# Kernel optimization log

Hardware: AMD Instinct MI355X
Metric: run time of the kernel (lower is better)

## Reference

```python
import jax, jax.numpy as jnp
import numpy as np

B, H, W, C = 16, 64, 64, 256
DIRECTIONS = [(0, -1), (1, -1), (1, 0), (1, 1), (0, 1), (-1, 1), (-1, 0), (-1, -1)]


def _shift(g, dx, dy):
    # zero-padded shift matching the torch _shift_grid semantics:
    # result[:, max(0,dy):H+min(0,dy), max(0,dx):W+min(0,dx)] = g[src slices]
    _, h, w, _ = g.shape
    padded = jnp.pad(g, ((0, 0), (max(0, dy), max(0, -dy)), (max(0, dx), max(0, -dx)), (0, 0)))
    return padded[:, max(0, -dy):max(0, -dy) + h, max(0, -dx):max(0, -dx) + w, :]


def setup_inputs() -> dict:
    key = jax.random.key(0)
    k1, k2, k3, k4 = jax.random.split(key, 4)
    grid_embedding = jax.random.normal(k1, (B, H, W, C), dtype=jnp.float32)
    Wd = jax.random.normal(k2, (8, C, C), dtype=jnp.float32) * 0.01  # per-direction weights
    Wc = jax.random.normal(k3, (C, 8 * C), dtype=jnp.float32) * 0.02  # Linear weight [out, in]
    bc = jax.random.normal(k4, (C,), dtype=jnp.float32) * 0.02
    return {"grid_embedding": grid_embedding, "Wd": Wd, "Wc": Wc, "bc": bc}


def reference(grid_embedding, Wd, Wc, bc):
    # stack the 8 zero-padded shifted copies: [8, B, H, W, C]
    shifted = jnp.stack([_shift(grid_embedding, dx, dy) for (dx, dy) in DIRECTIONS], axis=0)
    # per-direction channel matmul: [B, H, W, 8, C] (d-major over last two dims matches torch.cat order)
    proc = jnp.einsum('dbhwc,dce->bhwde', shifted, Wd)
    combined = proc.reshape(grid_embedding.shape[0], grid_embedding.shape[1], grid_embedding.shape[2], -1)
    # nn.Linear: y = x @ W.T + b
    return combined @ Wc.T + bc
```

## Files before the change

### kernel.cpp

```cpp
#include <hip/hip_runtime.h>


typedef unsigned short u16;
typedef unsigned int u32;
typedef __attribute__((ext_vector_type(8))) short bf16x8;
typedef __attribute__((ext_vector_type(4))) float f32x4;

#define GP_BYTES 35684352

__device__ __forceinline__ u16 f2bf(float f) {
  u32 u = __float_as_uint(f);
  u32 r = u + 0x7fffu + ((u >> 16) & 1u);
  return (u16)(r >> 16);
}
__device__ __forceinline__ u32 pack2(float a, float b) {
  return (u32)f2bf(a) | ((u32)f2bf(b) << 16);
}

__global__ __launch_bounds__(256) void pad_convert(const float* __restrict__ g,
                                                   u16* __restrict__ gp) {
  int id = blockIdx.x * 256 + threadIdx.x;
  if (id >= 2230272) return;
  int c8 = id & 31;
  int t = id >> 5;
  int xx = t % 66;
  int s = t / 66;
  int yy = s % 66;
  int b  = s / 66;
  u32 o0 = 0, o1 = 0, o2 = 0, o3 = 0;
  if (yy != 0 && yy != 65 && xx != 0 && xx != 65) {
    const float* src = g + ((((b << 6) + yy - 1) << 6) + xx - 1) * 256 + (c8 << 3);
    float4 fa = *(const float4*)src;
    float4 fb = *(const float4*)(src + 4);
    o0 = pack2(fa.x, fa.y);
    o1 = pack2(fa.z, fa.w);
    o2 = pack2(fb.x, fb.y);
    o3 = pack2(fb.z, fb.w);
  }
  uint4 v; v.x = o0; v.y = o1; v.z = o2; v.w = o3;
  *(uint4*)(gp + (size_t)id * 8) = v;
}

__global__ __launch_bounds__(256) void build_mt(const float* __restrict__ Wd,
                                                const float* __restrict__ Wc,
                                                u16* __restrict__ Bf) {
  __shared__ __align__(16) u16 As[128 * 32];
  __shared__ __align__(16) u16 Bs[128 * 32];
  const int bid = blockIdx.x;
  const int n0    = (bid & 1) << 7;
  const int mblk  = bid >> 1;
  const int d     = mblk >> 1;
  const int chalf = (mblk & 1) << 7;
  const int tid  = threadIdx.x;
  const int lane = tid & 63, wid = tid >> 6;
  const int wm = (wid >> 1) << 6, wn = (wid & 1) << 6;
  const int quad = lane >> 4, r16 = lane & 15;
  const int srow = tid >> 1, hh = tid & 1;
  const int swz  = (srow >> 1) & 3;
  const int ssl  = (quad ^ ((r16 >> 1) & 3)) << 3;
  f32x4 acc[4][4] = {};

  for (int e0 = 0; e0 < 256; e0 += 32) {
    __syncthreads();
    const float* pa = Wd + (size_t)(d * 256 + chalf + srow) * 256 + e0 + hh * 16;
    const float* pb = Wc + (size_t)(n0 + srow) * 2048 + d * 256 + e0 + hh * 16;
#pragma unroll
    for (int i = 0; i < 2; ++i) {
      float4 a0 = *(const float4*)(pa + i * 8);
      float4 a1 = *(const float4*)(pa + i * 8 + 4);
      float4 b0 = *(const float4*)(pb + i * 8);
      float4 b1 = *(const float4*)(pb + i * 8 + 4);
      uint4 va, vb;
      va.x = pack2(a0.x, a0.y); va.y = pack2(a0.z, a0.w);
      va.z = pack2(a1.x, a1.y); va.w = pack2(a1.z, a1.w);
      vb.x = pack2(b0.x, b0.y); vb.y = pack2(b0.z, b0.w);
      vb.z = pack2(b1.x, b1.y); vb.w = pack2(b1.z, b1.w);
      int slot = (2 * hh + i) ^ swz;
      *(uint4*)&As[srow * 32 + slot * 8] = va;
      *(uint4*)&Bs[srow * 32 + slot * 8] = vb;
    }
    __syncthreads();
    bf16x8 bfr[4];
#pragma unroll
    for (int nt = 0; nt < 4; ++nt)
      bfr[nt] = *(const bf16x8*)&Bs[(wn + nt * 16 + r16) * 32 + ssl];
#pragma unroll
    for (int mt = 0; mt < 4; ++mt) {
      bf16x8 af = *(const bf16x8*)&As[(wm + mt * 16 + r16) * 32 + ssl];
#pragma unroll
      for (int nt = 0; nt < 4; ++nt)
        acc[mt][nt] = __builtin_amdgcn_mfma_f32_16x16x32_bf16(af, bfr[nt], acc[mt][nt], 0, 0, 0);
    }
  }
#pragma unroll
  for (int mt = 0; mt < 4; ++mt) {
#pragma unroll
    for (int nt = 0; nt < 4; ++nt) {
      const int o = n0 + wn + nt * 16 + r16;
      f32x4 v = acc[mt][nt];
#pragma unroll
      for (int r = 0; r < 4; ++r) {
        const int c = chalf + wm + mt * 16 + quad * 4 + r;
        const int lane2 = (o & 15) + (((c >> 3) & 3) << 4);
        const size_t idx = ((size_t)((d * 8 + (c >> 5)) * 16 + (o >> 4)) * 512) + lane2 * 8 + (c & 7);
        Bf[idx] = f2bf(v[r]);
      }
    }
  }
}

__constant__ int DOFF[8] = {16896, 16640, -256, -17152, -16896, -16640, 256, 17152};

__device__ __forceinline__ void async16(const u16* g, u16* l) {
  __builtin_amdgcn_global_load_lds((const __attribute__((address_space(1))) u32*)g,
                                   (__attribute__((address_space(3))) u32*)l, 16, 0, 0);
}

__global__ __launch_bounds__(512, 2) void conv_gemm(const u16* __restrict__ gp,
                                                    const u16* __restrict__ Bf,
                                                    const float* __restrict__ bc,
                                                    float* __restrict__ out) {
  __shared__ __align__(16) u16 Asm[4][8192];
  const int bid = blockIdx.x;
  const int id2 = ((bid & 7) << 5) | (bid >> 3);
  const int b   = id2 >> 4;
  const int y0  = (id2 & 15) << 2;

  const int tid  = threadIdx.x;
  const int lane = tid & 63;
  const int wid  = tid >> 6;
  const int wm   = (wid >> 2) << 7;
  const int wn   = (wid & 3) << 6;
  const int quad = lane >> 4;
  const int r16  = lane & 15;

  const int chunk = (tid & 3) ^ ((tid >> 3) & 3);
  const u16* baseA = gp + ((b * 66 + y0 + 1 + (tid >> 8)) * 66 + ((tid >> 2) & 63) + 1) * 256
                        + (chunk << 3);
  const int ldso = tid * 8;

  const u16* baseBf = Bf + (wn >> 4) * 512 + lane * 8;

  const int ssl = (quad ^ ((r16 >> 1) & 3)) << 3;

  f32x4 acc[8][4] = {};
  bf16x8 bcur[4], bnxt[4];

  auto issueA = [&](int kt) {
    const int off = DOFF[kt >> 3] + ((kt & 7) << 5);
    async16(baseA + off,         Asm[kt & 3] + ldso);
    async16(baseA + off + 33792, Asm[kt & 3] + 4096 + ldso);
  };
  auto loadB = [&](int kt, bf16x8* dst) {
    const u16* bp = baseBf + (size_t)kt * 8192;
#pragma unroll
    for (int nt = 0; nt < 4; ++nt) dst[nt] = *(const bf16x8*)(bp + nt * 512);
  };
  auto readA = [&](int kt, bf16x8* af) {
    const u16* Ab = Asm[kt & 3];
#pragma unroll
    for (int mt = 0; mt < 8; ++mt)
      af[mt] = *(const bf16x8*)&Ab[(wm + mt * 16 + r16) * 32 + ssl];
  };
  auto domfma = [&](const bf16x8* af, const bf16x8* bb) {
    __builtin_amdgcn_s_setprio(1);
#pragma unroll
    for (int mt = 0; mt < 8; ++mt)
#pragma unroll
      for (int nt = 0; nt < 4; ++nt)
        acc[mt][nt] = __builtin_amdgcn_mfma_f32_16x16x32_bf16(af[mt], bb[nt], acc[mt][nt], 0, 0, 0);
    __builtin_amdgcn_s_setprio(0);
  };

  loadB(0, bcur);
  issueA(0);
  issueA(1);
  asm volatile("s_waitcnt vmcnt(2)" ::: "memory");
  asm volatile("s_barrier" ::: "memory");

#pragma unroll 2
  for (int kt = 0; kt < 62; ++kt) {
    loadB(kt + 1, bnxt);
    bf16x8 af[8];
    readA(kt, af);
    issueA(kt + 2);
    domfma(af, bcur);
    asm volatile("s_waitcnt vmcnt(2)" ::: "memory");
    asm volatile("s_barrier" ::: "memory");
#pragma unroll
    for (int nt = 0; nt < 4; ++nt) bcur[nt] = bnxt[nt];
  }
  {
    loadB(63, bnxt);
    bf16x8 af[8];
    readA(62, af);
    domfma(af, bcur);
    asm volatile("s_waitcnt vmcnt(0)" ::: "memory");
    asm volatile("s_barrier" ::: "memory");
#pragma unroll
    for (int nt = 0; nt < 4; ++nt) bcur[nt] = bnxt[nt];
  }
  {
    bf16x8 af[8];
    readA(63, af);
    domfma(af, bcur);
  }

  const int pbase = (b * 64 + y0) * 64;
#pragma unroll
  for (int nt = 0; nt < 4; ++nt) {
    const int o = wn + nt * 16 + r16;
    const float bias = bc[o];
#pragma unroll
    for (int mt = 0; mt < 8; ++mt) {
      const int pr = pbase + wm + mt * 16 + quad * 4;
      f32x4 v = acc[mt][nt];
#pragma unroll
      for (int r = 0; r < 4; ++r)
        out[(size_t)(pr + r) * 256 + o] = v[r] + bias;
    }
  }
}

extern "C" void kernel_launch(void* const* d_in, const int* in_sizes, int n_in,
                              void* d_out, int out_size, void* d_ws, size_t ws_size,
                              hipStream_t stream) {
  const float* g  = (const float*)d_in[0];
  const float* Wd = (const float*)d_in[1];
  const float* Wc = (const float*)d_in[2];
  const float* bc = (const float*)d_in[3];
  float* out = (float*)d_out;
  u16* gp = (u16*)d_ws;
  u16* Bf = (u16*)((char*)d_ws + GP_BYTES);

  pad_convert<<<8712, 256, 0, stream>>>(g, gp);
  build_mt<<<32, 256, 0, stream>>>(Wd, Wc, Bf);
  conv_gemm<<<256, 512, 0, stream>>>(gp, Bf, bc, out);
}
```

Baseline: 196.9 us.

## Stage B tiles through LDS with async loads and deepen prefetch to three

The GEMM kernel now copies each K-step's weight tile into a 4-slot LDS ring using asynchronous global-to-LDS loads, instead of having every wave load its B fragments from global memory into registers. A and B are both prefetched three stages ahead, and the vmcnt waits are adjusted to match. The aim is to drop the duplicated per-wave B loads, since waves that share a column slice no longer fetch it separately, and to hide more memory latency. The cost is doubled LDS use (128KB per block), which rules out two blocks per CU, plus extra LDS reads for B.

New measurement: 190.1 us. 3.4% less time.

```diff
diff --git a/kernel.cpp b/kernel.cpp
--- a/kernel.cpp
+++ b/kernel.cpp
@@ -121,6 +121,7 @@
                                                     const float* __restrict__ bc,
                                                     float* __restrict__ out) {
   __shared__ __align__(16) u16 Asm[4][8192];
+  __shared__ __align__(16) u16 Bsm[4][8192];
   const int bid = blockIdx.x;
   const int id2 = ((bid & 7) << 5) | (bid >> 3);
   const int b   = id2 >> 4;
@@ -139,28 +140,30 @@
                         + (chunk << 3);
   const int ldso = tid * 8;
 
-  const u16* baseBf = Bf + (wn >> 4) * 512 + lane * 8;
-
   const int ssl = (quad ^ ((r16 >> 1) & 3)) << 3;
 
   f32x4 acc[8][4] = {};
-  bf16x8 bcur[4], bnxt[4];
 
   auto issueA = [&](int kt) {
     const int off = DOFF[kt >> 3] + ((kt & 7) << 5);
     async16(baseA + off,         Asm[kt & 3] + ldso);
     async16(baseA + off + 33792, Asm[kt & 3] + 4096 + ldso);
   };
-  auto loadB = [&](int kt, bf16x8* dst) {
-    const u16* bp = baseBf + (size_t)kt * 8192;
-#pragma unroll
-    for (int nt = 0; nt < 4; ++nt) dst[nt] = *(const bf16x8*)(bp + nt * 512);
+  auto issueB = [&](int kt) {
+    const u16* src = Bf + (size_t)kt * 8192 + ldso;
+    async16(src,        Bsm[kt & 3] + ldso);
+    async16(src + 4096, Bsm[kt & 3] + 4096 + ldso);
   };
   auto readA = [&](int kt, bf16x8* af) {
     const u16* Ab = Asm[kt & 3];
 #pragma unroll
     for (int mt = 0; mt < 8; ++mt)
       af[mt] = *(const bf16x8*)&Ab[(wm + mt * 16 + r16) * 32 + ssl];
+  };
+  auto readB = [&](int kt, bf16x8* bb) {
+    const u16* Bb = Bsm[kt & 3] + ((wn >> 4) << 9) + lane * 8;
+#pragma unroll
+    for (int nt = 0; nt < 4; ++nt) bb[nt] = *(const bf16x8*)(Bb + nt * 512);
   };
   auto domfma = [&](const bf16x8* af, const bf16x8* bb) {
     __builtin_amdgcn_s_setprio(1);
@@ -172,38 +175,49 @@
     __builtin_amdgcn_s_setprio(0);
   };
 
-  loadB(0, bcur);
-  issueA(0);
-  issueA(1);
-  asm volatile("s_waitcnt vmcnt(2)" ::: "memory");
+  issueA(0); issueB(0);
+  issueA(1); issueB(1);
+  issueA(2); issueB(2);
+  asm volatile("s_waitcnt vmcnt(8)" ::: "memory");
   asm volatile("s_barrier" ::: "memory");
 
-#pragma unroll 2
-  for (int kt = 0; kt < 62; ++kt) {
-    loadB(kt + 1, bnxt);
-    bf16x8 af[8];
+#pragma unroll 4
+  for (int kt = 0; kt < 60; ++kt) {
+    bf16x8 bfr[4], af[8];
+    readB(kt, bfr);
     readA(kt, af);
-    issueA(kt + 2);
-    domfma(af, bcur);
-    asm volatile("s_waitcnt vmcnt(2)" ::: "memory");
-    asm volatile("s_barrier" ::: "memory");
-#pragma unroll
-    for (int nt = 0; nt < 4; ++nt) bcur[nt] = bnxt[nt];
-  }
-  {
-    loadB(63, bnxt);
-    bf16x8 af[8];
-    readA(62, af);
-    domfma(af, bcur);
+    issueA(kt + 3);
+    issueB(kt + 3);
+    domfma(af, bfr);
+    asm volatile("s_waitcnt vmcnt(8)" ::: "memory");
+    asm volatile("s_barrier" ::: "memory");
+  }
+  {
+    bf16x8 bfr[4], af[8];
+    readB(60, bfr); readA(60, af);
+    issueA(63); issueB(63);
+    domfma(af, bfr);
+    asm volatile("s_waitcnt vmcnt(8)" ::: "memory");
+    asm volatile("s_barrier" ::: "memory");
+  }
+  {
+    bf16x8 bfr[4], af[8];
+    readB(61, bfr); readA(61, af);
+    domfma(af, bfr);
+    asm volatile("s_waitcnt vmcnt(4)" ::: "memory");
+    asm volatile("s_barrier" ::: "memory");
+  }
+  {
+    bf16x8 bfr[4], af[8];
+    readB(62, bfr); readA(62, af);
+    domfma(af, bfr);
     asm volatile("s_waitcnt vmcnt(0)" ::: "memory");
     asm volatile("s_barrier" ::: "memory");
-#pragma unroll
-    for (int nt = 0; nt < 4; ++nt) bcur[nt] = bnxt[nt];
-  }
-  {
-    bf16x8 af[8];
-    readA(63, af);
-    domfma(af, bcur);
+  }
+  {
+    bf16x8 bfr[4], af[8];
+    readB(63, bfr); readA(63, af);
+    domfma(af, bfr);
   }
 
   const int pbase = (b * 64 + y0) * 64;
```

## Deepen conv GEMM pipeline to three A stages and split MFMA into halves

Applied to the files above, without the earlier changes.

The main loop now prefetches A tiles three steps ahead (using the 4-slot LDS ring) and B fragments two steps ahead with ping-pong register sets, which removes the per-iteration register copy of B. Each step's MFMA work is split into two halves so that LDS reads for the next half or step overlap with the current half's matrix ops. The intent is to hide global and LDS latency better, at the cost of more live registers, which could cut occupancy under the launch bound of 512 threads and 2 blocks.

Result: faster. 190.4 us (-3.3%).

```diff
diff --git a/kernel.cpp b/kernel.cpp
--- a/kernel.cpp
+++ b/kernel.cpp
@@ -139,12 +139,13 @@
                         + (chunk << 3);
   const int ldso = tid * 8;
 
-  const u16* baseBf = Bf + (wn >> 4) * 512 + lane * 8;
+  const u16* baseBf = Bf + ((wn >> 4) << 9) + lane * 8;
 
   const int ssl = (quad ^ ((r16 >> 1) & 3)) << 3;
 
   f32x4 acc[8][4] = {};
-  bf16x8 bcur[4], bnxt[4];
+  bf16x8 Be[4], Bo[4];
+  bf16x8 afl[4], afh[4];
 
   auto issueA = [&](int kt) {
     const int off = DOFF[kt >> 3] + ((kt & 7) << 5);
@@ -156,55 +157,55 @@
 #pragma unroll
     for (int nt = 0; nt < 4; ++nt) dst[nt] = *(const bf16x8*)(bp + nt * 512);
   };
-  auto readA = [&](int kt, bf16x8* af) {
+  auto readAh = [&](int kt, bf16x8* af, int h) {
     const u16* Ab = Asm[kt & 3];
 #pragma unroll
-    for (int mt = 0; mt < 8; ++mt)
-      af[mt] = *(const bf16x8*)&Ab[(wm + mt * 16 + r16) * 32 + ssl];
-  };
-  auto domfma = [&](const bf16x8* af, const bf16x8* bb) {
+    for (int mt = 0; mt < 4; ++mt)
+      af[mt] = *(const bf16x8*)&Ab[(wm + (h * 4 + mt) * 16 + r16) * 32 + ssl];
+  };
+  auto mfma_half = [&](const bf16x8* af, const bf16x8* bb, int h) {
     __builtin_amdgcn_s_setprio(1);
 #pragma unroll
-    for (int mt = 0; mt < 8; ++mt)
+    for (int mt = 0; mt < 4; ++mt)
 #pragma unroll
       for (int nt = 0; nt < 4; ++nt)
-        acc[mt][nt] = __builtin_amdgcn_mfma_f32_16x16x32_bf16(af[mt], bb[nt], acc[mt][nt], 0, 0, 0);
+        acc[h * 4 + mt][nt] =
+            __builtin_amdgcn_mfma_f32_16x16x32_bf16(af[mt], bb[nt], acc[h * 4 + mt][nt], 0, 0, 0);
     __builtin_amdgcn_s_setprio(0);
   };
 
-  loadB(0, bcur);
+  auto body = [&](int kt, bf16x8* bu, bool doB, bool doA, int vm) {
+    readAh(kt, afh, 1);
+    mfma_half(afl, bu, 0);
+    readAh(kt + 1, afl, 0);
+    mfma_half(afh, bu, 1);
+    if (doB) loadB(kt + 2, bu);
+    if (doA) issueA(kt + 3);
+    if (vm == 6)      asm volatile("s_waitcnt vmcnt(6)" ::: "memory");
+    else if (vm == 4) asm volatile("s_waitcnt vmcnt(4)" ::: "memory");
+    else              asm volatile("s_waitcnt vmcnt(0)" ::: "memory");
+    asm volatile("s_barrier" ::: "memory");
+  };
+
+  loadB(0, Be);
   issueA(0);
   issueA(1);
-  asm volatile("s_waitcnt vmcnt(2)" ::: "memory");
+  loadB(1, Bo);
+  issueA(2);
+  asm volatile("s_waitcnt vmcnt(6)" ::: "memory");
   asm volatile("s_barrier" ::: "memory");
-
-#pragma unroll 2
-  for (int kt = 0; kt < 62; ++kt) {
-    loadB(kt + 1, bnxt);
-    bf16x8 af[8];
-    readA(kt, af);
-    issueA(kt + 2);
-    domfma(af, bcur);
-    asm volatile("s_waitcnt vmcnt(2)" ::: "memory");
-    asm volatile("s_barrier" ::: "memory");
-#pragma unroll
-    for (int nt = 0; nt < 4; ++nt) bcur[nt] = bnxt[nt];
-  }
-  {
-    loadB(63, bnxt);
-    bf16x8 af[8];
-    readA(62, af);
-    domfma(af, bcur);
-    asm volatile("s_waitcnt vmcnt(0)" ::: "memory");
-    asm volatile("s_barrier" ::: "memory");
-#pragma unroll
-    for (int nt = 0; nt < 4; ++nt) bcur[nt] = bnxt[nt];
-  }
-  {
-    bf16x8 af[8];
-    readA(63, af);
-    domfma(af, bcur);
-  }
+  readAh(0, afl, 0);
+
+  for (int kt = 0; kt < 60; kt += 2) {
+    body(kt,     Be, true, true, 6);
+    body(kt + 1, Bo, true, true, 6);
+  }
+  body(60, Be, true,  true,  6);
+  body(61, Bo, true,  false, 4);
+  body(62, Be, false, false, 0);
+  readAh(63, afh, 1);
+  mfma_half(afl, Bo, 0);
+  mfma_half(afh, Bo, 1);
 
   const int pbase = (b * 64 + y0) * 64;
 #pragma unroll
```
